# Kernel optimization log

Measured on AMD Instinct MI355X. Metric: run time of the kernel, lower is better.

The kernel has to match this reference:

```python
import jax, jax.numpy as jnp
import numpy as np

N, E, D = 100000, 1600000, 128


def setup_inputs() -> dict:
    key = jax.random.key(0)
    ks = jax.random.split(key, 8)
    s = 1.0 / np.sqrt(D)
    return {
        "x": jax.random.normal(ks[0], (N, D), dtype=jnp.float32),
        "edge_index": jax.random.randint(ks[1], (2, E), 0, N, dtype=jnp.int64),
        "x_prev": jax.random.normal(ks[2], (N, D), dtype=jnp.float32),
        # GCNConv params: weight [in,out], bias [out]
        "W": jax.random.uniform(ks[3], (D, D), jnp.float32, -s, s),
        "b": jnp.zeros((D,), jnp.float32),
        # GRUCell params (torch layout): [3*H, H] gates ordered (r, z, n)
        "W_ih": jax.random.uniform(ks[4], (3 * D, D), jnp.float32, -s, s),
        "W_hh": jax.random.uniform(ks[5], (3 * D, D), jnp.float32, -s, s),
        "b_ih": jax.random.uniform(ks[6], (3 * D,), jnp.float32, -s, s),
        "b_hh": jax.random.uniform(ks[7], (3 * D,), jnp.float32, -s, s),
    }


def _gcn_conv(x, edge_index, W, b):
    n = x.shape[0]
    loop = jnp.arange(n, dtype=edge_index.dtype)
    src = jnp.concatenate([edge_index[0], loop])  # [E+N]
    dst = jnp.concatenate([edge_index[1], loop])
    # symmetric normalization: deg over destinations (incl. self loops)
    deg = jax.ops.segment_sum(jnp.ones_like(dst, dtype=x.dtype), dst, num_segments=n)
    dinv = jnp.where(deg > 0, jax.lax.rsqrt(deg), 0.0)
    norm = dinv[src] * dinv[dst]  # [E+N]
    xw = x @ W  # [N, out]
    msg = xw[src] * norm[:, None]  # gather + scale
    return jax.ops.segment_sum(msg, dst, num_segments=n) + b


def _gru_cell(inp, h, W_ih, W_hh, b_ih, b_hh):
    gi = inp @ W_ih.T + b_ih  # [N, 3H]
    gh = h @ W_hh.T + b_hh
    i_r, i_z, i_n = jnp.split(gi, 3, axis=-1)
    h_r, h_z, h_n = jnp.split(gh, 3, axis=-1)
    r = jax.nn.sigmoid(i_r + h_r)
    z = jax.nn.sigmoid(i_z + h_z)
    ntil = jnp.tanh(i_n + r * h_n)
    return (1.0 - z) * ntil + z * h


def reference(x, edge_index, x_prev, W, b, W_ih, W_hh, b_ih, b_hh):
    h_cur = _gcn_conv(x, edge_index, W, b)
    return _gru_cell(h_cur, x_prev, W_ih, W_hh, b_ih, b_hh)
```

## Files before the change

### kernel.cpp

```cpp
#include <hip/hip_runtime.h>
#include <hip/hip_bf16.h>
#include <math.h>

#define DIM 128
#define PSHIFT 10
#define PSZ 1024
#define CHUNK 4096

typedef __attribute__((ext_vector_type(8))) short bf16x8;
typedef __attribute__((ext_vector_type(4))) float f32x4;
typedef __attribute__((ext_vector_type(2))) float f32x2;
typedef unsigned short u16;
typedef unsigned char u8;
typedef unsigned int u32;
typedef unsigned long long u64;

__device__ __forceinline__ u16 f2bf(float x) {
    u32 u = __builtin_bit_cast(u32, x);
    u += 0x7fff + ((u >> 16) & 1);
    return (u16)(u >> 16);
}
__device__ __forceinline__ float bf2f(u16 h) {
    return __builtin_bit_cast(float, (u32)h << 16);
}
__device__ __forceinline__ float fsig(float x) {
    return __builtin_amdgcn_rcpf(1.f + __expf(-x));
}
__device__ __forceinline__ float ftanh(float x) {
    return 1.f - 2.f * __builtin_amdgcn_rcpf(__expf(2.f * x) + 1.f);
}
__device__ __forceinline__ u8 f2fp8(float v) {
    int pk = __builtin_amdgcn_cvt_pk_fp8_f32(v, v, 0, false);
    return (u8)(pk & 0xff);
}


__global__ __launch_bounds__(256) void k_prepcount(const int* __restrict__ edst,
                                                   int* __restrict__ pcnt, int E,
                                                   const float* __restrict__ W,
                                                   const float* __restrict__ Wih,
                                                   const float* __restrict__ Whh,
                                                   const float4* __restrict__ xp,
                                                   u16* __restrict__ Wt,
                                                   u16* __restrict__ Wihb,
                                                   u16* __restrict__ Whhb,
                                                   u32* __restrict__ Xpb, int n4) {
    __shared__ int h[128];
    int t = threadIdx.x;
    int gid = blockIdx.x * 256 + t;
    int stride = gridDim.x * 256;
    if (t < 128) h[t] = 0;
    __syncthreads();
    for (int e = gid; e < E; e += stride)
        atomicAdd(&h[edst[e] >> PSHIFT], 1);
    for (int i = gid; i < n4; i += stride) {
        float4 v = xp[i];
        Xpb[i * 2 + 0] = (u32)f2bf(v.x) | ((u32)f2bf(v.y) << 16);
        Xpb[i * 2 + 1] = (u32)f2bf(v.z) | ((u32)f2bf(v.w) << 16);
    }
    if (gid < 128 * 128) {
        int k = gid >> 7, c = gid & 127;
        Wt[c * 128 + k] = f2bf(W[gid]);
    }
    if (gid < 3 * 128 * 128) {
        Wihb[gid] = f2bf(Wih[gid]);
        Whhb[gid] = f2bf(Whh[gid]);
    }
    __syncthreads();
    if (t < 128 && h[t]) atomicAdd(&pcnt[t], h[t]);
}

__global__ __launch_bounds__(256) void k_pscan(const int* __restrict__ pcnt,
                                               int* __restrict__ poff,
                                               int* __restrict__ pfill,
                                               int* __restrict__ rowp,
                                               int P, int N, int E) {
    __shared__ int a[256];
    int t = threadIdx.x;
    int v = (t < P) ? pcnt[t] : 0;
    a[t] = v;
    __syncthreads();
    #pragma unroll
    for (int off = 1; off < 256; off <<= 1) {
        int y = (t >= off) ? a[t - off] : 0;
        __syncthreads();
        a[t] += y;
        __syncthreads();
    }
    int excl = a[t] - v;
    if (t < P) { poff[t] = excl; pfill[t] = excl; }
    if (t == 0) { poff[P] = E; rowp[N] = E; }
}

__global__ __launch_bounds__(256) void k_pscatter(const int* __restrict__ esrc,
                                                  const int* __restrict__ edst,
                                                  int* __restrict__ pfill,
                                                  u64* __restrict__ pbuf, int E) {
    __shared__ int hist[128], sc[128], lofs[128], gbase[128];
    __shared__ u32 ss[CHUNK], sd[CHUNK];
    int t = threadIdx.x;
    int c0 = blockIdx.x * CHUNK;
    int cnt = E - c0; if (cnt > CHUNK) cnt = CHUNK;

    if (t < 128) hist[t] = 0;
    __syncthreads();

    u32 s[16], d[16];
    int p[16], r[16];
    #pragma unroll
    for (int j = 0; j < 16; ++j) {
        int i = j * 256 + t;
        if (i < cnt) {
            s[j] = (u32)esrc[c0 + i];
            d[j] = (u32)edst[c0 + i];
            p[j] = (int)(d[j] >> PSHIFT);
            r[j] = atomicAdd(&hist[p[j]], 1);
        }
    }
    __syncthreads();

    if (t < 128) sc[t] = hist[t];
    __syncthreads();
    #pragma unroll
    for (int off = 1; off < 128; off <<= 1) {
        int y = 0;
        if (t < 128 && t >= off) y = sc[t - off];
        __syncthreads();
        if (t < 128) sc[t] += y;
        __syncthreads();
    }
    if (t < 128) {
        lofs[t] = sc[t] - hist[t];
        if (hist[t] > 0) gbase[t] = atomicAdd(&pfill[t], hist[t]);
    }
    __syncthreads();

    #pragma unroll
    for (int j = 0; j < 16; ++j) {
        int i = j * 256 + t;
        if (i < cnt) {
            int idx = lofs[p[j]] + r[j];
            ss[idx] = s[j];
            sd[idx] = d[j];
        }
    }
    __syncthreads();

    for (int i = t; i < cnt; i += 256) {
        u32 dd = sd[i];
        int pp = (int)(dd >> PSHIFT);
        int gpos = gbase[pp] + (i - lofs[pp]);
        pbuf[gpos] = (u64)ss[i] | ((u64)dd << 32);
    }
}

__global__ __launch_bounds__(256) void k_pfill(const u64* __restrict__ pbuf,
                                               const int* __restrict__ poff,
                                               int* __restrict__ rowp,
                                               int* __restrict__ srcs,
                                               float* __restrict__ dinv, int N) {
    __shared__ int cnt[PSZ];
    __shared__ int wsum[4];
    int p = blockIdx.x, t = threadIdx.x;
    int lane = t & 63, wid = t >> 6;
    int nb0 = p << PSHIFT;
    int ncnt = N - nb0; if (ncnt > PSZ) ncnt = PSZ;
    int b0 = poff[p], b1 = poff[p + 1];
    int bc = b1 - b0;

    for (int i = t; i < PSZ; i += 256) cnt[i] = 0;
    __syncthreads();
    for (int i = t; i < bc; i += 256) {
        u32 d = (u32)(pbuf[b0 + i] >> 32);
        atomicAdd(&cnt[d - nb0], 1);
    }
    __syncthreads();

    int base = t * 4;
    int c[4];
    int ssum = 0;
    #pragma unroll
    for (int j = 0; j < 4; ++j) { c[j] = cnt[base + j]; ssum += c[j]; }
    int incl = ssum;
    #pragma unroll
    for (int off = 1; off < 64; off <<= 1) {
        int y = __shfl_up(incl, off, 64);
        if (lane >= off) incl += y;
    }
    if (lane == 63) wsum[wid] = incl;
    __syncthreads();
    int add = 0;
    for (int w = 0; w < wid; ++w) add += wsum[w];
    int rr = b0 + add + (incl - ssum);
    #pragma unroll
    for (int j = 0; j < 4; ++j) {
        int i = base + j;
        if (i < ncnt) {
            rowp[nb0 + i] = rr;
            dinv[nb0 + i] = rsqrtf((float)(c[j] + 1));
        }
        cnt[i] = rr;
        rr += c[j];
    }
    __syncthreads();

    for (int i = t; i < bc; i += 256) {
        u64 v = pbuf[b0 + i];
        u32 sv = (u32)v;
        u32 d = (u32)(v >> 32);
        int pos = atomicAdd(&cnt[d - nb0], 1);
        srcs[pos] = (int)sv;
    }
}


__global__ __launch_bounds__(256) void k_gemm1(const float* __restrict__ X,
                                               const u16* __restrict__ Wt,
                                               const float* __restrict__ dinv,
                                               u8* __restrict__ XW8, int n) {
    __shared__ u16 Wlds[128 * 128];
    int t = threadIdx.x, w = t >> 6, l = t & 63;
    int lr = l & 15, q = l >> 4;

    for (int cidx = t; cidx < 2048; cidx += 256) {
        int r = cidx >> 4, kc = cidx & 15;
        int dst = r * 128 + ((kc * 8) ^ ((r & 7) << 3));
        *(bf16x8*)(Wlds + dst) = *(const bf16x8*)(Wt + r * 128 + kc * 8);
    }
    __syncthreads();

    int r0 = blockIdx.x * 128;
    int wrow0 = r0 + w * 32;
    int sw = (lr & 7) << 3;
    int ar0 = wrow0 + lr;      if (ar0 > n - 1) ar0 = n - 1;
    int ar1 = wrow0 + 16 + lr; if (ar1 > n - 1) ar1 = n - 1;
    const float* x0 = X + (size_t)ar0 * DIM;
    const float* x1 = X + (size_t)ar1 * DIM;

    f32x4 acc[2][8];
    #pragma unroll
    for (int s = 0; s < 2; ++s)
        #pragma unroll
        for (int c = 0; c < 8; ++c) acc[s][c] = (f32x4){0.f, 0.f, 0.f, 0.f};

    #pragma unroll
    for (int kb = 0; kb < 4; ++kb) {
        int ko = kb * 32 + q * 8;
        float4 f00 = *(const float4*)(x0 + ko), f01 = *(const float4*)(x0 + ko + 4);
        float4 f10 = *(const float4*)(x1 + ko), f11 = *(const float4*)(x1 + ko + 4);
        bf16x8 a0, a1;
        a0[0] = (short)f2bf(f00.x); a0[1] = (short)f2bf(f00.y);
        a0[2] = (short)f2bf(f00.z); a0[3] = (short)f2bf(f00.w);
        a0[4] = (short)f2bf(f01.x); a0[5] = (short)f2bf(f01.y);
        a0[6] = (short)f2bf(f01.z); a0[7] = (short)f2bf(f01.w);
        a1[0] = (short)f2bf(f10.x); a1[1] = (short)f2bf(f10.y);
        a1[2] = (short)f2bf(f10.z); a1[3] = (short)f2bf(f10.w);
        a1[4] = (short)f2bf(f11.x); a1[5] = (short)f2bf(f11.y);
        a1[6] = (short)f2bf(f11.z); a1[7] = (short)f2bf(f11.w);
        int kw = ko ^ sw;
        #pragma unroll
        for (int ct = 0; ct < 8; ++ct) {
            bf16x8 b = *(const bf16x8*)(Wlds + (ct * 16 + lr) * 128 + kw);
            acc[0][ct] = __builtin_amdgcn_mfma_f32_16x16x32_bf16(a0, b, acc[0][ct], 0, 0, 0);
            acc[1][ct] = __builtin_amdgcn_mfma_f32_16x16x32_bf16(a1, b, acc[1][ct], 0, 0, 0);
        }
    }

    float dv[2][4];
    #pragma unroll
    for (int s = 0; s < 2; ++s)
        #pragma unroll
        for (int i = 0; i < 4; ++i) {
            int row = wrow0 + s * 16 + q * 4 + i; if (row > n - 1) row = n - 1;
            dv[s][i] = dinv[row];
        }
    #pragma unroll
    for (int s = 0; s < 2; ++s)
        #pragma unroll
        for (int ct = 0; ct < 8; ++ct)
            #pragma unroll
            for (int i = 0; i < 4; ++i) {
                int row = wrow0 + s * 16 + q * 4 + i;
                if (row < n)
                    XW8[(size_t)row * DIM + ct * 16 + lr] = f2fp8(acc[s][ct][i] * dv[s][i]);
            }
}


__global__ __launch_bounds__(256) void k_gather(const u8* __restrict__ XW8,
                                                const float* __restrict__ dinv,
                                                const int* __restrict__ row_ptr,
                                                const int* __restrict__ srcs,
                                                const float* __restrict__ bias,
                                                u16* __restrict__ Hcb, int n) {
    int node = blockIdx.x * 4 + (threadIdx.x >> 6);
    if (node >= n) return;
    int lane = threadIdx.x & 63;
    int c = lane * 2;

    u16 sv = *(const u16*)(XW8 + (size_t)node * DIM + c);
    f32x2 sf = __builtin_amdgcn_cvt_pk_f32_fp8((int)(u32)sv, false);
    float accx = sf[0], accy = sf[1];

    int e = row_ptr[node], end = row_ptr[node + 1];
    for (; e + 7 < end; e += 8) {
        int sdx[8]; u16 vv[8];
        #pragma unroll
        for (int j = 0; j < 8; ++j) sdx[j] = srcs[e + j];
        #pragma unroll
        for (int j = 0; j < 8; ++j)
            vv[j] = *(const u16*)(XW8 + (size_t)sdx[j] * DIM + c);
        #pragma unroll
        for (int j = 0; j < 8; ++j) {
            f32x2 f = __builtin_amdgcn_cvt_pk_f32_fp8((int)(u32)vv[j], false);
            accx += f[0];
            accy += f[1];
        }
    }
    for (; e < end; ++e) {
        u16 v = *(const u16*)(XW8 + (size_t)srcs[e] * DIM + c);
        f32x2 f = __builtin_amdgcn_cvt_pk_f32_fp8((int)(u32)v, false);
        accx += f[0];
        accy += f[1];
    }
    float di = dinv[node];
    float ox = accx * di + bias[c];
    float oy = accy * di + bias[c + 1];
    *(u32*)(Hcb + (size_t)node * DIM + c) = (u32)f2bf(ox) | ((u32)f2bf(oy) << 16);
}


__global__ __launch_bounds__(256) void k_gru(const u16* __restrict__ Hcb,
                                             const u16* __restrict__ Xpb,
                                             const u16* __restrict__ Wihb,
                                             const u16* __restrict__ Whhb,
                                             const float* __restrict__ bih,
                                             const float* __restrict__ bhh,
                                             float* __restrict__ Out, int n) {
    __shared__ u16 Wlds[96 * 128];
    int t = threadIdx.x, w = t >> 6, l = t & 63;
    int lr = l & 15, q = l >> 4;

    int nwg = gridDim.x;
    int qq = nwg >> 3, rr8 = nwg & 7;
    int xcd = blockIdx.x & 7, idx = blockIdx.x >> 3;
    int logical = (xcd < rr8 ? xcd * (qq + 1) : rr8 * (qq + 1) + (xcd - rr8) * qq) + idx;
    int cs = logical & 7;
    int rb = logical >> 3;
    int c0 = cs * 16;
    int r0 = rb * 128;

    for (int cidx = t; cidx < 1536; cidx += 256) {
        int r = cidx >> 4, kc = cidx & 15;
        int m = (r >= 48);
        int rr = m ? r - 48 : r;
        int g = rr >> 4, cc = rr & 15;
        const u16* src = (m ? Whhb : Wihb) + (size_t)((g << 7) + c0 + cc) * DIM + kc * 8;
        int dst = r * 128 + ((kc * 8) ^ ((r & 7) << 3));
        *(bf16x8*)(Wlds + dst) = *(const bf16x8*)src;
    }
    __syncthreads();

    int wrow0 = r0 + w * 32;
    int sw = (lr & 7) << 3;
    int ar0 = wrow0 + lr;      if (ar0 > n - 1) ar0 = n - 1;
    int ar1 = wrow0 + 16 + lr; if (ar1 > n - 1) ar1 = n - 1;
    const u16* hb0 = Hcb + (size_t)ar0 * DIM;
    const u16* hb1 = Hcb + (size_t)ar1 * DIM;
    const u16* xb0 = Xpb + (size_t)ar0 * DIM;
    const u16* xb1 = Xpb + (size_t)ar1 * DIM;

    f32x4 aI[3][2], aH[3][2];
    #pragma unroll
    for (int g = 0; g < 3; ++g)
        #pragma unroll
        for (int s = 0; s < 2; ++s) {
            aI[g][s] = (f32x4){0.f, 0.f, 0.f, 0.f};
            aH[g][s] = (f32x4){0.f, 0.f, 0.f, 0.f};
        }

    #pragma unroll
    for (int kb = 0; kb < 4; ++kb) {
        int ko = kb * 32 + q * 8;
        bf16x8 hA0 = *(const bf16x8*)(hb0 + ko);
        bf16x8 hA1 = *(const bf16x8*)(hb1 + ko);
        bf16x8 xA0 = *(const bf16x8*)(xb0 + ko);
        bf16x8 xA1 = *(const bf16x8*)(xb1 + ko);
        int kw = ko ^ sw;
        #pragma unroll
        for (int g = 0; g < 3; ++g) {
            int ridx = (g * 16 + lr) * 128 + kw;
            bf16x8 bI = *(const bf16x8*)(Wlds + ridx);
            bf16x8 bH = *(const bf16x8*)(Wlds + ridx + 48 * 128);
            aI[g][0] = __builtin_amdgcn_mfma_f32_16x16x32_bf16(hA0, bI, aI[g][0], 0, 0, 0);
            aI[g][1] = __builtin_amdgcn_mfma_f32_16x16x32_bf16(hA1, bI, aI[g][1], 0, 0, 0);
            aH[g][0] = __builtin_amdgcn_mfma_f32_16x16x32_bf16(xA0, bH, aH[g][0], 0, 0, 0);
            aH[g][1] = __builtin_amdgcn_mfma_f32_16x16x32_bf16(xA1, bH, aH[g][1], 0, 0, 0);
        }
    }

    int j = c0 + lr;
    float br = bih[j],       bz = bih[128 + j], bn = bih[256 + j];
    float cr = bhh[j],       cz = bhh[128 + j], cn = bhh[256 + j];
    #pragma unroll
    for (int s = 0; s < 2; ++s)
        #pragma unroll
        for (int i = 0; i < 4; ++i) {
            int row = wrow0 + s * 16 + q * 4 + i;
            if (row >= n) continue;
            float ir = aI[0][s][i] + br;
            float iz = aI[1][s][i] + bz;
            float in_ = aI[2][s][i] + bn;
            float hr = aH[0][s][i] + cr;
            float hz = aH[1][s][i] + cz;
            float hn = aH[2][s][i] + cn;
            float rg = fsig(ir + hr);
            float zc = fsig(-(iz + hz));
            float ng = ftanh(in_ + rg * hn);
            float hp = bf2f((u16)Xpb[(size_t)row * DIM + j]);
            Out[(size_t)row * DIM + j] = fmaf(zc, ng - hp, hp);
        }
}


extern "C" void kernel_launch(void* const* d_in, const int* in_sizes, int n_in,
                              void* d_out, int out_size, void* d_ws, size_t ws_size,
                              hipStream_t stream) {
    const float* x     = (const float*)d_in[0];
    const int*   ei    = (const int*)d_in[1];
    const float* xprev = (const float*)d_in[2];
    const float* W     = (const float*)d_in[3];
    const float* b     = (const float*)d_in[4];
    const float* Wih   = (const float*)d_in[5];
    const float* Whh   = (const float*)d_in[6];
    const float* bih   = (const float*)d_in[7];
    const float* bhh   = (const float*)d_in[8];

    int N = in_sizes[0] / DIM;
    int E = in_sizes[1] / 2;
    int P = (N + PSZ - 1) >> PSHIFT;
    const int* esrc = ei;
    const int* edst = ei + E;

    char* p = (char*)d_ws;
    auto alloc = [&](size_t bytes) {
        char* q = p;
        p += (bytes + 255) & ~(size_t)255;
        return q;
    };
    float* dinv = (float*)alloc((size_t)N * 4);
    int*   rowp = (int*)  alloc((size_t)(N + 1) * 4);
    int*   srcs = (int*)  alloc((size_t)E * 4);
    u16*   Hcb  = (u16*)  alloc((size_t)N * DIM * 2);
    u16*   Xpb  = (u16*)  alloc((size_t)N * DIM * 2);
    size_t xwsz = (size_t)N * DIM;
    size_t pbsz = (size_t)E * 8;
    u8*    XW8  = (u8*)   alloc(xwsz > pbsz ? xwsz : pbsz);
    u16*   Wt   = (u16*)  alloc(128 * 128 * 2);
    u16*   Wihb = (u16*)  alloc(3 * 128 * 128 * 2);
    u16*   Whhb = (u16*)  alloc(3 * 128 * 128 * 2);
    int*   pcnt = (int*)  alloc(128 * 4);
    int*   poff = (int*)  alloc(129 * 4);
    int*   pfil = (int*)  alloc(128 * 4);
    u64*   pbuf = (u64*)XW8;
    float* out  = (float*)d_out;

    hipMemsetAsync(pcnt, 0, 128 * 4, stream);
    int n4 = N * DIM / 4;
    k_prepcount<<<2048, 256, 0, stream>>>(edst, pcnt, E, W, Wih, Whh,
                                          (const float4*)xprev,
                                          Wt, Wihb, Whhb, (u32*)Xpb, n4);
    k_pscan   <<<1, 256, 0, stream>>>(pcnt, poff, pfil, rowp, P, N, E);
    int nch = (E + CHUNK - 1) / CHUNK;
    k_pscatter<<<nch, 256, 0, stream>>>(esrc, edst, pfil, pbuf, E);
    k_pfill   <<<P, 256, 0, stream>>>(pbuf, poff, rowp, srcs, dinv, N);
    int nrb = (N + 127) / 128;
    k_gemm1   <<<nrb, 256, 0, stream>>>(x, Wt, dinv, XW8, N);
    k_gather  <<<(N + 3) / 4, 256, 0, stream>>>(XW8, dinv, rowp, srcs, b, Hcb, N);
    k_gru     <<<nrb * 8, 256, 0, stream>>>(Hcb, Xpb, Wihb, Whhb, bih, bhh, out, N);
}
```

Measured before the change: 277.4 us.

## Pack partition buffer entries into 32 bits and process two row tiles per GRU block

The edge partition buffer now stores each edge as a single 32-bit word (source shifted left plus the low bits of the destination) instead of a 64-bit pair. This halves the buffer traffic in the scatter and fill kernels and shrinks the scatter kernel's shared memory. The scatter kernel now finds each entry's partition with a binary search over the local offsets. The GRU kernel processes 256 rows per block in two 128-row passes, so each block's weight slice staged in LDS is reused twice and half as many blocks are launched. Packing assumes node ids fit in 22 bits, and a leftover empty loop remains in the scatter kernel.

```diff
diff --git a/kernel.cpp b/kernel.cpp
--- a/kernel.cpp
+++ b/kernel.cpp
@@ -95,9 +95,9 @@
 __global__ __launch_bounds__(256) void k_pscatter(const int* __restrict__ esrc,
                                                   const int* __restrict__ edst,
                                                   int* __restrict__ pfill,
-                                                  u64* __restrict__ pbuf, int E) {
+                                                  u32* __restrict__ pbuf, int E) {
     __shared__ int hist[128], sc[128], lofs[128], gbase[128];
-    __shared__ u32 ss[CHUNK], sd[CHUNK];
+    __shared__ u32 sp[CHUNK];
     int t = threadIdx.x;
     int c0 = blockIdx.x * CHUNK;
     int cnt = E - c0; if (cnt > CHUNK) cnt = CHUNK;
@@ -140,21 +140,32 @@
         int i = j * 256 + t;
         if (i < cnt) {
             int idx = lofs[p[j]] + r[j];
-            ss[idx] = s[j];
-            sd[idx] = d[j];
-        }
-    }
-    __syncthreads();
-
+            sp[idx] = (s[j] << PSHIFT) | (d[j] & (PSZ - 1));
+        }
+    }
+    __syncthreads();
+
+    #pragma unroll
+    for (int j = 0; j < 16; ++j) {
+        int i = j * 256 + t;
+        if (i < cnt) {
+            int idx = lofs[p[j]] + r[j];
+        }
+    }
     for (int i = t; i < cnt; i += 256) {
-        u32 dd = sd[i];
-        int pp = (int)(dd >> PSHIFT);
+        int lo = 0, hi = 127;
+        #pragma unroll
+        for (int step = 0; step < 7; ++step) {
+            int mid = (lo + hi + 1) >> 1;
+            if (lofs[mid] <= i) lo = mid; else hi = mid - 1;
+        }
+        int pp = lo;
         int gpos = gbase[pp] + (i - lofs[pp]);
-        pbuf[gpos] = (u64)ss[i] | ((u64)dd << 32);
-    }
-}
-
-__global__ __launch_bounds__(256) void k_pfill(const u64* __restrict__ pbuf,
+        pbuf[gpos] = sp[i];
+    }
+}
+
+__global__ __launch_bounds__(256) void k_pfill(const u32* __restrict__ pbuf,
                                                const int* __restrict__ poff,
                                                int* __restrict__ rowp,
                                                int* __restrict__ srcs,
@@ -171,8 +182,8 @@
     for (int i = t; i < PSZ; i += 256) cnt[i] = 0;
     __syncthreads();
     for (int i = t; i < bc; i += 256) {
-        u32 d = (u32)(pbuf[b0 + i] >> 32);
-        atomicAdd(&cnt[d - nb0], 1);
+        u32 ld = pbuf[b0 + i] & (PSZ - 1);
+        atomicAdd(&cnt[ld], 1);
     }
     __syncthreads();
 
@@ -205,11 +216,10 @@
     __syncthreads();
 
     for (int i = t; i < bc; i += 256) {
-        u64 v = pbuf[b0 + i];
-        u32 sv = (u32)v;
-        u32 d = (u32)(v >> 32);
-        int pos = atomicAdd(&cnt[d - nb0], 1);
-        srcs[pos] = (int)sv;
+        u32 v = pbuf[b0 + i];
+        u32 ld = v & (PSZ - 1);
+        int pos = atomicAdd(&cnt[ld], 1);
+        srcs[pos] = (int)(v >> PSHIFT);
     }
 }
 
@@ -348,7 +358,7 @@
     int cs = logical & 7;
     int rb = logical >> 3;
     int c0 = cs * 16;
-    int r0 = rb * 128;
+    int r0 = rb * 256;
 
     for (int cidx = t; cidx < 1536; cidx += 256) {
         int r = cidx >> 4, kc = cidx & 15;
@@ -361,65 +371,70 @@
     }
     __syncthreads();
 
-    int wrow0 = r0 + w * 32;
     int sw = (lr & 7) << 3;
-    int ar0 = wrow0 + lr;      if (ar0 > n - 1) ar0 = n - 1;
-    int ar1 = wrow0 + 16 + lr; if (ar1 > n - 1) ar1 = n - 1;
-    const u16* hb0 = Hcb + (size_t)ar0 * DIM;
-    const u16* hb1 = Hcb + (size_t)ar1 * DIM;
-    const u16* xb0 = Xpb + (size_t)ar0 * DIM;
-    const u16* xb1 = Xpb + (size_t)ar1 * DIM;
-
-    f32x4 aI[3][2], aH[3][2];
-    #pragma unroll
-    for (int g = 0; g < 3; ++g)
-        #pragma unroll
-        for (int s = 0; s < 2; ++s) {
-            aI[g][s] = (f32x4){0.f, 0.f, 0.f, 0.f};
-            aH[g][s] = (f32x4){0.f, 0.f, 0.f, 0.f};
-        }
-
-    #pragma unroll
-    for (int kb = 0; kb < 4; ++kb) {
-        int ko = kb * 32 + q * 8;
-        bf16x8 hA0 = *(const bf16x8*)(hb0 + ko);
-        bf16x8 hA1 = *(const bf16x8*)(hb1 + ko);
-        bf16x8 xA0 = *(const bf16x8*)(xb0 + ko);
-        bf16x8 xA1 = *(const bf16x8*)(xb1 + ko);
-        int kw = ko ^ sw;
-        #pragma unroll
-        for (int g = 0; g < 3; ++g) {
-            int ridx = (g * 16 + lr) * 128 + kw;
-            bf16x8 bI = *(const bf16x8*)(Wlds + ridx);
-            bf16x8 bH = *(const bf16x8*)(Wlds + ridx + 48 * 128);
-            aI[g][0] = __builtin_amdgcn_mfma_f32_16x16x32_bf16(hA0, bI, aI[g][0], 0, 0, 0);
-            aI[g][1] = __builtin_amdgcn_mfma_f32_16x16x32_bf16(hA1, bI, aI[g][1], 0, 0, 0);
-            aH[g][0] = __builtin_amdgcn_mfma_f32_16x16x32_bf16(xA0, bH, aH[g][0], 0, 0, 0);
-            aH[g][1] = __builtin_amdgcn_mfma_f32_16x16x32_bf16(xA1, bH, aH[g][1], 0, 0, 0);
-        }
-    }
-
     int j = c0 + lr;
     float br = bih[j],       bz = bih[128 + j], bn = bih[256 + j];
     float cr = bhh[j],       cz = bhh[128 + j], cn = bhh[256 + j];
-    #pragma unroll
-    for (int s = 0; s < 2; ++s)
-        #pragma unroll
-        for (int i = 0; i < 4; ++i) {
-            int row = wrow0 + s * 16 + q * 4 + i;
-            if (row >= n) continue;
-            float ir = aI[0][s][i] + br;
-            float iz = aI[1][s][i] + bz;
-            float in_ = aI[2][s][i] + bn;
-            float hr = aH[0][s][i] + cr;
-            float hz = aH[1][s][i] + cz;
-            float hn = aH[2][s][i] + cn;
-            float rg = fsig(ir + hr);
-            float zc = fsig(-(iz + hz));
-            float ng = ftanh(in_ + rg * hn);
-            float hp = bf2f((u16)Xpb[(size_t)row * DIM + j]);
-            Out[(size_t)row * DIM + j] = fmaf(zc, ng - hp, hp);
-        }
+
+    #pragma unroll 1
+    for (int half = 0; half < 2; ++half) {
+        int wrow0 = r0 + half * 128 + w * 32;
+        if (wrow0 >= n) break;
+        int ar0 = wrow0 + lr;      if (ar0 > n - 1) ar0 = n - 1;
+        int ar1 = wrow0 + 16 + lr; if (ar1 > n - 1) ar1 = n - 1;
+        const u16* hb0 = Hcb + (size_t)ar0 * DIM;
+        const u16* hb1 = Hcb + (size_t)ar1 * DIM;
+        const u16* xb0 = Xpb + (size_t)ar0 * DIM;
+        const u16* xb1 = Xpb + (size_t)ar1 * DIM;
+
+        f32x4 aI[3][2], aH[3][2];
+        #pragma unroll
+        for (int g = 0; g < 3; ++g)
+            #pragma unroll
+            for (int s = 0; s < 2; ++s) {
+                aI[g][s] = (f32x4){0.f, 0.f, 0.f, 0.f};
+                aH[g][s] = (f32x4){0.f, 0.f, 0.f, 0.f};
+            }
+
+        #pragma unroll
+        for (int kb = 0; kb < 4; ++kb) {
+            int ko = kb * 32 + q * 8;
+            bf16x8 hA0 = *(const bf16x8*)(hb0 + ko);
+            bf16x8 hA1 = *(const bf16x8*)(hb1 + ko);
+            bf16x8 xA0 = *(const bf16x8*)(xb0 + ko);
+            bf16x8 xA1 = *(const bf16x8*)(xb1 + ko);
+            int kw = ko ^ sw;
+            #pragma unroll
+            for (int g = 0; g < 3; ++g) {
+                int ridx = (g * 16 + lr) * 128 + kw;
+                bf16x8 bI = *(const bf16x8*)(Wlds + ridx);
+                bf16x8 bH = *(const bf16x8*)(Wlds + ridx + 48 * 128);
+                aI[g][0] = __builtin_amdgcn_mfma_f32_16x16x32_bf16(hA0, bI, aI[g][0], 0, 0, 0);
+                aI[g][1] = __builtin_amdgcn_mfma_f32_16x16x32_bf16(hA1, bI, aI[g][1], 0, 0, 0);
+                aH[g][0] = __builtin_amdgcn_mfma_f32_16x16x32_bf16(xA0, bH, aH[g][0], 0, 0, 0);
+                aH[g][1] = __builtin_amdgcn_mfma_f32_16x16x32_bf16(xA1, bH, aH[g][1], 0, 0, 0);
+            }
+        }
+
+        #pragma unroll
+        for (int s = 0; s < 2; ++s)
+            #pragma unroll
+            for (int i = 0; i < 4; ++i) {
+                int row = wrow0 + s * 16 + q * 4 + i;
+                if (row >= n) continue;
+                float ir = aI[0][s][i] + br;
+                float iz = aI[1][s][i] + bz;
+                float in_ = aI[2][s][i] + bn;
+                float hr = aH[0][s][i] + cr;
+                float hz = aH[1][s][i] + cz;
+                float hn = aH[2][s][i] + cn;
+                float rg = fsig(ir + hr);
+                float zc = fsig(-(iz + hz));
+                float ng = ftanh(in_ + rg * hn);
+                float hp = bf2f((u16)Xpb[(size_t)row * DIM + j]);
+                Out[(size_t)row * DIM + j] = fmaf(zc, ng - hp, hp);
+            }
+    }
 }
 
 
@@ -454,7 +469,7 @@
     u16*   Hcb  = (u16*)  alloc((size_t)N * DIM * 2);
     u16*   Xpb  = (u16*)  alloc((size_t)N * DIM * 2);
     size_t xwsz = (size_t)N * DIM;
-    size_t pbsz = (size_t)E * 8;
+    size_t pbsz = (size_t)E * 4;
     u8*    XW8  = (u8*)   alloc(xwsz > pbsz ? xwsz : pbsz);
     u16*   Wt   = (u16*)  alloc(128 * 128 * 2);
     u16*   Wihb = (u16*)  alloc(3 * 128 * 128 * 2);
@@ -462,7 +477,7 @@
     int*   pcnt = (int*)  alloc(128 * 4);
     int*   poff = (int*)  alloc(129 * 4);
     int*   pfil = (int*)  alloc(128 * 4);
-    u64*   pbuf = (u64*)XW8;
+    u32*   pbuf = (u32*)XW8;
     float* out  = (float*)d_out;
 
     hipMemsetAsync(pcnt, 0, 128 * 4, stream);
@@ -477,5 +492,6 @@
     int nrb = (N + 127) / 128;
     k_gemm1   <<<nrb, 256, 0, stream>>>(x, Wt, dinv, XW8, N);
     k_gather  <<<(N + 3) / 4, 256, 0, stream>>>(XW8, dinv, rowp, srcs, b, Hcb, N);
-    k_gru     <<<nrb * 8, 256, 0, stream>>>(Hcb, Xpb, Wihb, Whhb, bih, bhh, out, N);
-}
+    int ngb = (N + 255) / 256;
+    k_gru     <<<ngb * 8, 256, 0, stream>>>(Hcb, Xpb, Wihb, Whhb, bih, bhh, out, N);
+}
```

Result: faster. 270.9 us (-2.3%).
